# Kernel optimization log

Hardware: AMD Instinct MI355X
Metric: run time of the kernel (lower is better)

## Reference

```python
import jax, jax.numpy as jnp
import numpy as np

TEMP = 0.07
EPS = 1e-8
THRESH = 0.0          # self.global_threshold default
NORM_EPS = 1e-12      # F.normalize default eps


def setup_inputs() -> dict:
    key = jax.random.key(0)
    k1, k2, k3 = jax.random.split(key, 3)
    T, C, H, W = 8, 256, 64, 64
    return {
        "current_preds": jax.random.uniform(k1, (T, 1, H, W), jnp.float32),
        "history_preds": jax.random.uniform(k2, (T, 1, H, W), jnp.float32),
        "features": jax.random.normal(k3, (T, C, H, W), jnp.float32),
        "epoch": 1,
    }


def _supervised_labels(current_preds, history_preds):
    # Deviation per video (Dice-like metrics on binarized preds), then select
    # current pred if dev <= threshold else history pred (both detached).
    T = current_preds.shape[0]
    cb = (current_preds > 0.5).astype(jnp.float32).reshape(T, -1)
    hb = (history_preds > 0.5).astype(jnp.float32).reshape(T, -1)
    e1 = (cb * hb).sum(axis=1)
    e2 = cb.sum(axis=1) + hb.sum(axis=1)
    m1 = (2.0 * e1 + EPS) / (e2 + EPS)
    m2 = (e1 + EPS) / (e2 - e1 + EPS)
    dev = 1.0 - (m1 + m2) / 2.0                       # [T]
    use_curr = (dev <= THRESH)[:, None, None, None]
    return jnp.where(use_curr, current_preds, history_preds)


def _contrastive_loss(features, labels):
    T, C, H, W = features.shape
    N = H * W
    feat = features.reshape(T, C, N).transpose(0, 2, 1)            # [T,N,C]
    nrm = jnp.linalg.norm(feat, axis=-1, keepdims=True)
    feat = feat / jnp.maximum(nrm, NORM_EPS)                       # L2 normalize
    lbl = labels.reshape(T, N)
    fg = lbl > 0.5
    bg = ~fg
    sim = jnp.einsum('tnc,tmc->tnm', feat, feat) / TEMP            # [T,N,N]
    pos = jnp.exp(jnp.diagonal(sim, axis1=1, axis2=2))             # [T,N]
    # neg_i = sum over bg columns of exp(sim); masked matvec honors fg/bg split
    neg = jnp.einsum('tnm,tm->tn', jnp.exp(sim), bg.astype(feat.dtype))
    per_pix = -jnp.log(pos / (pos + neg + EPS))                    # [T,N]
    fgf = fg.astype(feat.dtype)
    n_fg = fgf.sum(axis=1)
    frame_loss = (per_pix * fgf).sum(axis=1) / jnp.maximum(n_fg, 1.0)  # mean over fg
    valid = (fg.any(axis=1) & bg.any(axis=1)).astype(feat.dtype)   # frames with both
    n_valid = valid.sum()
    return jnp.where(n_valid > 0,
                     (frame_loss * valid).sum() / jnp.maximum(n_valid, 1.0),
                     jnp.zeros((), feat.dtype))


def reference(current_preds, history_preds, features, epoch):
    # epoch >= 1 path of DOC.forward (epoch==0 only populates memory)
    labels = jax.lax.stop_gradient(_supervised_labels(current_preds, history_preds))
    loss = _contrastive_loss(features, labels)
    return (labels, loss)
```

## Files before the change

kernel.cpp:

```cpp
#include <hip/hip_runtime.h>
#include <hip/hip_bf16.h>
#include <cstdint>
#include <cstddef>

constexpr int T = 8;
constexpr int C = 256;
constexpr int N = 4096;
constexpr float TEMP_INV = 14.285714285714286f;
constexpr float EPS = 1e-8f;

typedef __bf16 bf16;
typedef __bf16 bf16x8 __attribute__((ext_vector_type(8)));
typedef float floatx4 __attribute__((ext_vector_type(4)));

__device__ __forceinline__ void async_copy16(const bf16* g, bf16* l) {
    __builtin_amdgcn_global_load_lds((const __attribute__((address_space(1))) void*)g,
                                     (__attribute__((address_space(3))) void*)l,
                                     16, 0, 0);
}

__global__ void prep_kernel(const float* __restrict__ cur,
                            const float* __restrict__ hist,
                            float* __restrict__ out_labels,
                            float* __restrict__ negbuf,
                            unsigned short* __restrict__ fgidx,
                            unsigned short* __restrict__ bgidx,
                            int* __restrict__ nfg, int* __restrict__ nbg) {
    int t = blockIdx.x;
    int tid = threadIdx.x;
    int lane = tid & 63;
    int w = tid >> 6;

    float cv[4], hv[4];
    float s1 = 0.f, sc = 0.f, sh = 0.f;
    #pragma unroll
    for (int it = 0; it < 4; ++it) {
        int p = it * 1024 + tid;
        float c = cur[t * N + p];
        float h = hist[t * N + p];
        cv[it] = c; hv[it] = h;
        float cb = c > 0.5f ? 1.f : 0.f;
        float hb = h > 0.5f ? 1.f : 0.f;
        s1 += cb * hb; sc += cb; sh += hb;
    }
    for (int o = 32; o > 0; o >>= 1) {
        s1 += __shfl_down(s1, o);
        sc += __shfl_down(sc, o);
        sh += __shfl_down(sh, o);
    }
    __shared__ float r1[16], r2[16], r3[16];
    __shared__ float uflag;
    __shared__ int cfg_s, cbg_s;
    if (lane == 0) { r1[w] = s1; r2[w] = sc; r3[w] = sh; }
    if (tid == 0) { cfg_s = 0; cbg_s = 0; }
    __syncthreads();
    if (tid == 0) {
        float e1 = 0.f, scs = 0.f, shs = 0.f;
        for (int i = 0; i < 16; ++i) { e1 += r1[i]; scs += r2[i]; shs += r3[i]; }
        float e2 = scs + shs;
        float m1 = (2.f * e1 + EPS) / (e2 + EPS);
        float m2 = (e1 + EPS) / (e2 - e1 + EPS);
        float dev = 1.f - 0.5f * (m1 + m2);
        uflag = (dev <= 0.0f) ? 1.f : 0.f;
    }
    __syncthreads();
    bool use_curr = uflag != 0.f;
    for (int it = 0; it < 4; ++it) {
        int p = it * 1024 + tid;
        int gi = t * N + p;
        float lab = use_curr ? cv[it] : hv[it];
        out_labels[gi] = lab;
        negbuf[gi] = 0.f;
        bool fg = lab > 0.5f;
        unsigned long long b = __ballot(fg);
        unsigned long long lowmask = (lane == 63) ? 0x7fffffffffffffffull
                                                  : ((1ull << lane) - 1ull);
        int rank_fg = __popcll(b & lowmask);
        int rank_bg = __popcll((~b) & lowmask);
        int cnt_fg = __popcll(b);
        int base_fg = 0, base_bg = 0;
        if (lane == 0) {
            base_fg = atomicAdd(&cfg_s, cnt_fg);
            base_bg = atomicAdd(&cbg_s, 64 - cnt_fg);
        }
        base_fg = __shfl(base_fg, 0);
        base_bg = __shfl(base_bg, 0);
        if (fg) fgidx[t * N + base_fg + rank_fg] = (unsigned short)p;
        else    bgidx[t * N + base_bg + rank_bg] = (unsigned short)p;
    }
    __syncthreads();
    if (tid == 0) { nfg[t] = cfg_s; nbg[t] = cbg_s; }
}

__global__ __launch_bounds__(256, 4) void normalize_kernel(const float* __restrict__ feat,
                                                           bf16* __restrict__ fhat,
                                                           float* __restrict__ posdot) {
    __shared__ bf16 tile[64 * 258];
    __shared__ float partial[256];
    __shared__ float rnorm_s[64];
    int t = blockIdx.x >> 6;
    int n0 = (blockIdx.x & 63) * 64;
    int tid = threadIdx.x;
    int lane63 = tid & 63;
    int w = tid >> 6;
    const float* fb = feat + (size_t)t * C * N;
    float ss = 0.f;
    #pragma unroll 16
    for (int it = 0; it < 64; ++it) {
        int c = w * 64 + it;
        float v = fb[(size_t)c * N + n0 + lane63];
        ss += v * v;
        tile[lane63 * 258 + c] = (bf16)v;
    }
    partial[tid] = ss;
    __syncthreads();
    if (tid < 64) {
        float s = partial[tid] + partial[tid + 64] + partial[tid + 128] + partial[tid + 192];
        float r = 1.f / fmaxf(sqrtf(s), 1e-12f);
        rnorm_s[tid] = r;
        posdot[t * N + n0 + tid] = s * r * r;
    }
    __syncthreads();
    bf16* ob = fhat + ((size_t)t * N + n0) * C;
    #pragma unroll
    for (int it = 0; it < 8; ++it) {
        int l = it * 256 + tid;
        int n = l >> 5;
        int c = (l & 31) * 8;
        float r = rnorm_s[n];
        bf16x8 vin = *(const bf16x8*)&tile[n * 258 + c];
        bf16x8 vo;
        for (int j = 0; j < 8; ++j) vo[j] = (bf16)((float)vin[j] * r);
        *(bf16x8*)(ob + l * 8) = vo;
    }
}

__global__ __launch_bounds__(256, 3) void sim_kernel(const bf16* __restrict__ fhat,
                                                     const unsigned short* __restrict__ fgidx,
                                                     const unsigned short* __restrict__ bgidx,
                                                     const int* __restrict__ nfg,
                                                     const int* __restrict__ nbg,
                                                     float* __restrict__ neg) {
    int t = blockIdx.x & 7;
    int tile = blockIdx.x >> 3;
    int rowbase = (tile >> 5) * 128;
    int colbase = (tile & 31) * 128;
    int nfgt = nfg[t];
    int nbgt = nbg[t];
    if (rowbase >= nfgt || colbase >= nbgt) return;

    __shared__ bf16 a_lds[128 * 64];
    __shared__ bf16 b_lds[128 * 64];
    int tid = threadIdx.x;
    int lane = tid & 63;
    int w = tid >> 6;
    const bf16* fb = fhat + (size_t)t * N * C;

    int ch = (lane & 7) ^ (lane >> 3);
    int r0w = (w & 1) * 64;
    int c0w = (w >> 1) * 64;

    const bf16* arp[4];
    const bf16* brp[4];
    for (int s = 0; s < 4; ++s) {
        int q = w * 4 + s;
        int row_l = q * 8 + (lane >> 3);
        int ra = rowbase + row_l; if (ra >= nfgt) ra = nfgt - 1;
        int rb = colbase + row_l; if (rb >= nbgt) rb = nbgt - 1;
        arp[s] = fb + (size_t)fgidx[t * N + ra] * C + ch * 8;
        brp[s] = fb + (size_t)bgidx[t * N + rb] * C + ch * 8;
    }

    floatx4 acc[4][4];
    for (int i = 0; i < 4; ++i)
        for (int j = 0; j < 4; ++j)
            acc[i][j] = (floatx4){0.f, 0.f, 0.f, 0.f};

    for (int ks = 0; ks < 4; ++ks) {
        int k0 = ks * 64;
        __syncthreads();
        for (int s = 0; s < 4; ++s) {
            int q = w * 4 + s;
            async_copy16(arp[s] + k0, &a_lds[q * 512]);
            async_copy16(brp[s] + k0, &b_lds[q * 512]);
        }
        __syncthreads();
        for (int kk = 0; kk < 64; kk += 32) {
            int quad = lane >> 4;
            int chread = (kk >> 3) + quad;
            bf16x8 af[4], bfr[4];
            for (int i = 0; i < 4; ++i) {
                int r = r0w + 16 * i + (lane & 15);
                int chs = chread ^ (r & 7);
                af[i] = *(const bf16x8*)&a_lds[r * 64 + chs * 8];
            }
            for (int j = 0; j < 4; ++j) {
                int cidx = c0w + 16 * j + (lane & 15);
                int chs = chread ^ (cidx & 7);
                bfr[j] = *(const bf16x8*)&b_lds[cidx * 64 + chs * 8];
            }
            for (int i = 0; i < 4; ++i)
                for (int j = 0; j < 4; ++j)
                    acc[i][j] = __builtin_amdgcn_mfma_f32_16x16x32_bf16(af[i], bfr[j], acc[i][j], 0, 0, 0);
        }
    }

    float bgv[4];
    for (int j = 0; j < 4; ++j) {
        int cidx = colbase + c0w + 16 * j + (lane & 15);
        bgv[j] = (cidx < nbgt) ? 1.f : 0.f;
    }

    int quad = lane >> 4;
    for (int i = 0; i < 4; ++i) {
        for (int reg = 0; reg < 4; ++reg) {
            float msum = 0.f;
            for (int j = 0; j < 4; ++j)
                msum += __expf(acc[i][j][reg] * TEMP_INV) * bgv[j];
            msum += __shfl_xor(msum, 1);
            msum += __shfl_xor(msum, 2);
            msum += __shfl_xor(msum, 4);
            msum += __shfl_xor(msum, 8);
            if ((lane & 15) == 0) {
                int row = rowbase + r0w + 16 * i + quad * 4 + reg;
                if (row < nfgt) atomicAdd(&neg[t * N + row], msum);
            }
        }
    }
}

__global__ void loss_kernel(const float* __restrict__ negbuf,
                            const float* __restrict__ posdot,
                            const unsigned short* __restrict__ fgidx,
                            const int* __restrict__ nfg,
                            const int* __restrict__ nbg,
                            float* __restrict__ out_loss) {
    int tid = threadIdx.x;
    int t = tid >> 6;
    int lane = tid & 63;
    int nfgt = nfg[t];
    float s = 0.f;
    #pragma unroll 4
    for (int k = lane; k < nfgt; k += 64) {
        int pix = fgidx[t * N + k];
        float pos = __expf(posdot[t * N + pix] * TEMP_INV);
        float ng = negbuf[t * N + k];
        s += logf((pos + ng + EPS) / pos);
    }
    for (int o = 32; o > 0; o >>= 1) s += __shfl_down(s, o);
    __shared__ float fl[8], vv[8];
    if (lane == 0) {
        float valid = (nfgt > 0 && nbg[t] > 0) ? 1.f : 0.f;
        fl[t] = valid * (s / fmaxf((float)nfgt, 1.f));
        vv[t] = valid;
    }
    __syncthreads();
    if (tid == 0) {
        float ls = 0.f, v = 0.f;
        for (int i = 0; i < T; ++i) { ls += fl[i]; v += vv[i]; }
        out_loss[0] = (v > 0.f) ? ls / fmaxf(v, 1.f) : 0.f;
    }
}

extern "C" void kernel_launch(void* const* d_in, const int* in_sizes, int n_in,
                              void* d_out, int out_size, void* d_ws, size_t ws_size,
                              hipStream_t stream) {
    const float* cur  = (const float*)d_in[0];
    const float* hist = (const float*)d_in[1];
    const float* feat = (const float*)d_in[2];
    float* out = (float*)d_out;

    char* ws = (char*)d_ws;
    bf16*  fhat    = (bf16*)ws;
    float* negbuf  = (float*)(ws + 16777216);
    float* posdot  = (float*)(ws + 16908288);
    unsigned short* fgidx = (unsigned short*)(ws + 17039360);
    unsigned short* bgidx = (unsigned short*)(ws + 17104896);
    int*   nfg     = (int*)(ws + 17170432);
    int*   nbg     = nfg + 8;

    prep_kernel<<<8, 1024, 0, stream>>>(cur, hist, out, negbuf, fgidx, bgidx, nfg, nbg);
    normalize_kernel<<<512, 256, 0, stream>>>(feat, fhat, posdot);
    sim_kernel<<<8192, 256, 0, stream>>>(fhat, fgidx, bgidx, nfg, nbg, negbuf);
    loss_kernel<<<1, 512, 0, stream>>>(negbuf, posdot, fgidx, nfg, nbg, out + 32768);
}
```

Measured before the change: 153.5 us.

## Pack normalized features by fg/bg rank to drop gather indirection in sim kernel

The prep kernel now writes a per-pixel rank map (fg flag plus rank) instead of separate fg/bg index lists. The normalize kernel uses it to scatter each normalized bf16 row into a packed buffer, fg rows first and then bg rows from an 8-aligned base, with the LDS XOR swizzle already applied. This lets the sim kernel load contiguous rows directly, without the index loads and random gathers. Padding rows at the end are zeroed so tile overruns read finite data. The cost is scattered writes in normalize and a larger workspace.

```diff
diff --git a/kernel.cpp b/kernel.cpp
--- a/kernel.cpp
+++ b/kernel.cpp
@@ -6,6 +6,7 @@
 constexpr int T = 8;
 constexpr int C = 256;
 constexpr int N = 4096;
+constexpr int CAP = 4232;
 constexpr float TEMP_INV = 14.285714285714286f;
 constexpr float EPS = 1e-8f;
 
@@ -23,8 +24,8 @@
                             const float* __restrict__ hist,
                             float* __restrict__ out_labels,
                             float* __restrict__ negbuf,
-                            unsigned short* __restrict__ fgidx,
-                            unsigned short* __restrict__ bgidx,
+                            unsigned short* __restrict__ rankmap,
+                            bf16* __restrict__ fpack,
                             int* __restrict__ nfg, int* __restrict__ nbg) {
     int t = blockIdx.x;
     int tid = threadIdx.x;
@@ -85,24 +86,34 @@
         }
         base_fg = __shfl(base_fg, 0);
         base_bg = __shfl(base_bg, 0);
-        if (fg) fgidx[t * N + base_fg + rank_fg] = (unsigned short)p;
-        else    bgidx[t * N + base_bg + rank_bg] = (unsigned short)p;
+        int rank = fg ? (base_fg + rank_fg) : (base_bg + rank_bg);
+        rankmap[gi] = (unsigned short)(rank | (fg ? 0x8000 : 0));
     }
     __syncthreads();
     if (tid == 0) { nfg[t] = cfg_s; nbg[t] = cbg_s; }
+    float4 z4 = make_float4(0.f, 0.f, 0.f, 0.f);
+    float4* pz = (float4*)(fpack + ((size_t)t * CAP + N) * C);
+    int chunks = (CAP - N) * (C / 8);
+    for (int i = tid; i < chunks; i += 1024) pz[i] = z4;
 }
 
 __global__ __launch_bounds__(256, 4) void normalize_kernel(const float* __restrict__ feat,
-                                                           bf16* __restrict__ fhat,
-                                                           float* __restrict__ posdot) {
+                                                           const unsigned short* __restrict__ rankmap,
+                                                           const int* __restrict__ nfg,
+                                                           bf16* __restrict__ fpack,
+                                                           float* __restrict__ posc) {
     __shared__ bf16 tile[64 * 258];
     __shared__ float partial[256];
     __shared__ float rnorm_s[64];
+    __shared__ unsigned short rk_s[64];
+    __shared__ int bbase_s;
     int t = blockIdx.x >> 6;
     int n0 = (blockIdx.x & 63) * 64;
     int tid = threadIdx.x;
     int lane63 = tid & 63;
     int w = tid >> 6;
+    if (tid == 0) bbase_s = (nfg[t] + 7) & ~7;
+    if (tid < 64) rk_s[tid] = rankmap[t * N + n0 + tid];
     const float* fb = feat + (size_t)t * C * N;
     float ss = 0.f;
     #pragma unroll 16
@@ -118,26 +129,29 @@
         float s = partial[tid] + partial[tid + 64] + partial[tid + 128] + partial[tid + 192];
         float r = 1.f / fmaxf(sqrtf(s), 1e-12f);
         rnorm_s[tid] = r;
-        posdot[t * N + n0 + tid] = s * r * r;
-    }
-    __syncthreads();
-    bf16* ob = fhat + ((size_t)t * N + n0) * C;
+        unsigned short rk = rk_s[tid];
+        if (rk & 0x8000) posc[t * N + (rk & 0x7fff)] = s * r * r;
+    }
+    __syncthreads();
+    int bbase = bbase_s;
+    bf16* fp = fpack + (size_t)t * CAP * C;
     #pragma unroll
     for (int it = 0; it < 8; ++it) {
         int l = it * 256 + tid;
         int n = l >> 5;
-        int c = (l & 31) * 8;
+        int c8 = l & 31;
+        unsigned short rk = rk_s[n];
+        int r_pack = (rk & 0x7fff) + ((rk & 0x8000) ? 0 : bbase);
+        int slot = (c8 & ~7) | ((c8 & 7) ^ (r_pack & 7));
         float r = rnorm_s[n];
-        bf16x8 vin = *(const bf16x8*)&tile[n * 258 + c];
+        bf16x8 vin = *(const bf16x8*)&tile[n * 258 + c8 * 8];
         bf16x8 vo;
         for (int j = 0; j < 8; ++j) vo[j] = (bf16)((float)vin[j] * r);
-        *(bf16x8*)(ob + l * 8) = vo;
-    }
-}
-
-__global__ __launch_bounds__(256, 3) void sim_kernel(const bf16* __restrict__ fhat,
-                                                     const unsigned short* __restrict__ fgidx,
-                                                     const unsigned short* __restrict__ bgidx,
+        *(bf16x8*)(fp + (size_t)r_pack * C + slot * 8) = vo;
+    }
+}
+
+__global__ __launch_bounds__(256, 3) void sim_kernel(const bf16* __restrict__ fpack,
                                                      const int* __restrict__ nfg,
                                                      const int* __restrict__ nbg,
                                                      float* __restrict__ neg) {
@@ -148,28 +162,19 @@
     int nfgt = nfg[t];
     int nbgt = nbg[t];
     if (rowbase >= nfgt || colbase >= nbgt) return;
+    int bbase = (nfgt + 7) & ~7;
 
     __shared__ bf16 a_lds[128 * 64];
     __shared__ bf16 b_lds[128 * 64];
     int tid = threadIdx.x;
     int lane = tid & 63;
     int w = tid >> 6;
-    const bf16* fb = fhat + (size_t)t * N * C;
-
-    int ch = (lane & 7) ^ (lane >> 3);
+    const bf16* fb = fpack + (size_t)t * CAP * C;
+
+    int lrow = lane >> 3;
+    int lchunk = lane & 7;
     int r0w = (w & 1) * 64;
     int c0w = (w >> 1) * 64;
-
-    const bf16* arp[4];
-    const bf16* brp[4];
-    for (int s = 0; s < 4; ++s) {
-        int q = w * 4 + s;
-        int row_l = q * 8 + (lane >> 3);
-        int ra = rowbase + row_l; if (ra >= nfgt) ra = nfgt - 1;
-        int rb = colbase + row_l; if (rb >= nbgt) rb = nbgt - 1;
-        arp[s] = fb + (size_t)fgidx[t * N + ra] * C + ch * 8;
-        brp[s] = fb + (size_t)bgidx[t * N + rb] * C + ch * 8;
-    }
 
     floatx4 acc[4][4];
     for (int i = 0; i < 4; ++i)
@@ -181,8 +186,10 @@
         __syncthreads();
         for (int s = 0; s < 4; ++s) {
             int q = w * 4 + s;
-            async_copy16(arp[s] + k0, &a_lds[q * 512]);
-            async_copy16(brp[s] + k0, &b_lds[q * 512]);
+            int ra = rowbase + q * 8 + lrow;
+            int rb = bbase + colbase + q * 8 + lrow;
+            async_copy16(fb + (size_t)ra * C + k0 + lchunk * 8, &a_lds[q * 512]);
+            async_copy16(fb + (size_t)rb * C + k0 + lchunk * 8, &b_lds[q * 512]);
         }
         __syncthreads();
         for (int kk = 0; kk < 64; kk += 32) {
@@ -210,7 +217,6 @@
         int cidx = colbase + c0w + 16 * j + (lane & 15);
         bgv[j] = (cidx < nbgt) ? 1.f : 0.f;
     }
-
     int quad = lane >> 4;
     for (int i = 0; i < 4; ++i) {
         for (int reg = 0; reg < 4; ++reg) {
@@ -230,8 +236,7 @@
 }
 
 __global__ void loss_kernel(const float* __restrict__ negbuf,
-                            const float* __restrict__ posdot,
-                            const unsigned short* __restrict__ fgidx,
+                            const float* __restrict__ posc,
                             const int* __restrict__ nfg,
                             const int* __restrict__ nbg,
                             float* __restrict__ out_loss) {
@@ -242,8 +247,7 @@
     float s = 0.f;
     #pragma unroll 4
     for (int k = lane; k < nfgt; k += 64) {
-        int pix = fgidx[t * N + k];
-        float pos = __expf(posdot[t * N + pix] * TEMP_INV);
+        float pos = __expf(posc[t * N + k] * TEMP_INV);
         float ng = negbuf[t * N + k];
         s += logf((pos + ng + EPS) / pos);
     }
@@ -271,16 +275,16 @@
     float* out = (float*)d_out;
 
     char* ws = (char*)d_ws;
-    bf16*  fhat    = (bf16*)ws;
-    float* negbuf  = (float*)(ws + 16777216);
-    float* posdot  = (float*)(ws + 16908288);
-    unsigned short* fgidx = (unsigned short*)(ws + 17039360);
-    unsigned short* bgidx = (unsigned short*)(ws + 17104896);
-    int*   nfg     = (int*)(ws + 17170432);
+    bf16*  fpack   = (bf16*)ws;
+    size_t off = (size_t)T * CAP * C * sizeof(bf16);
+    float* negbuf  = (float*)(ws + off);  off += (size_t)T * N * 4;
+    float* posc    = (float*)(ws + off);  off += (size_t)T * N * 4;
+    unsigned short* rankmap = (unsigned short*)(ws + off); off += (size_t)T * N * 2;
+    int*   nfg     = (int*)(ws + off);
     int*   nbg     = nfg + 8;
 
-    prep_kernel<<<8, 1024, 0, stream>>>(cur, hist, out, negbuf, fgidx, bgidx, nfg, nbg);
-    normalize_kernel<<<512, 256, 0, stream>>>(feat, fhat, posdot);
-    sim_kernel<<<8192, 256, 0, stream>>>(fhat, fgidx, bgidx, nfg, nbg, negbuf);
-    loss_kernel<<<1, 512, 0, stream>>>(negbuf, posdot, fgidx, nfg, nbg, out + 32768);
-}
+    prep_kernel<<<8, 1024, 0, stream>>>(cur, hist, out, negbuf, rankmap, fpack, nfg, nbg);
+    normalize_kernel<<<512, 256, 0, stream>>>(feat, rankmap, nfg, fpack, posc);
+    sim_kernel<<<8192, 256, 0, stream>>>(fpack, nfg, nbg, negbuf);
+    loss_kernel<<<1, 512, 0, stream>>>(negbuf, posc, nfg, nbg, out + 32768);
+}
```

Result: faster. 149.1 us (-2.9%).
